# Performance work log

Measured on AMD Instinct MI355X. Metric: run time of the kernel, lower is better.

## Reference

```python
import jax, jax.numpy as jnp
import numpy as np

N_NODES = 20000
N_EDGES = 640000
D = 128            # node feature dim
NUM_HEADS = 4      # = num_irreps of edge_sh (lmax=3, 0e+1o+2e+3o)
HEAD_DIM = D // NUM_HEADS
IR_DIMS = np.array([1, 3, 5, 7])  # dims of each irrep; sum = 16
AVG_NUM_NEIGHBORS = 32.0


def setup_inputs() -> dict:
    key = jax.random.key(0)
    ks = jax.random.split(key, 20)
    inp = {
        "edge_sh": jax.random.normal(ks[0], (N_EDGES, int(IR_DIMS.sum())), jnp.float32),
        "node_feats": jax.random.normal(ks[1], (N_NODES, D), jnp.float32),
        "edge_feats": jax.random.normal(ks[2], (N_EDGES, 64), jnp.float32),
        "chi_scalar": jax.random.normal(ks[3], (N_EDGES, 64), jnp.float32),
        "cutoffs": jax.random.uniform(ks[4], (N_EDGES,), jnp.float32),
        "senders": jax.random.randint(ks[5], (N_EDGES,), 0, N_NODES),
        "receivers": jax.random.randint(ks[6], (N_EDGES,), 0, N_NODES),
        # radial MLP: 64 -> 128 -> 128 (silu between)
        "W_rad1": jax.random.normal(ks[7], (64, 128), jnp.float32) / np.sqrt(64),
        "b_rad1": jnp.zeros((128,), jnp.float32),
        "W_rad2": jax.random.normal(ks[8], (128, 128), jnp.float32) / np.sqrt(128),
        "b_rad2": jnp.zeros((128,), jnp.float32),
        # spherical-scalar MLP: 64 -> 128 -> 128
        "W_sph1": jax.random.normal(ks[9], (64, 128), jnp.float32) / np.sqrt(64),
        "b_sph1": jnp.zeros((128,), jnp.float32),
        "W_sph2": jax.random.normal(ks[10], (128, 128), jnp.float32) / np.sqrt(128),
        "b_sph2": jnp.zeros((128,), jnp.float32),
        # Q/K projections, no bias
        "Wq": jax.random.normal(ks[11], (D, D), jnp.float32) / np.sqrt(D),
        "Wk": jax.random.normal(ks[12], (D, D), jnp.float32) / np.sqrt(D),
    }
    return inp


def reference(edge_sh, node_feats, edge_feats, chi_scalar, cutoffs, senders,
              receivers, W_rad1, b_rad1, W_rad2, b_rad2, W_sph1, b_sph1,
              W_sph2, b_sph2, Wq, Wk):
    silu = jax.nn.silu
    # edge filter: radial MLP + spherical-scalar MLP
    w = silu(edge_feats @ W_rad1 + b_rad1) @ W_rad2 + b_rad2      # [E, D]
    w = w + (silu(chi_scalar @ W_sph1 + b_sph1) @ W_sph2 + b_sph2)
    w = w.reshape(-1, NUM_HEADS, HEAD_DIM)                        # [E, H, hd]
    # gathered queries/keys
    q = (node_feats @ Wq).reshape(-1, NUM_HEADS, HEAD_DIM)[receivers]
    k = (node_feats @ Wk).reshape(-1, NUM_HEADS, HEAD_DIM)[senders]
    # filter-scaled attention: per-edge, per-head scalar
    alpha = (q * w * k).sum(axis=-1) * (1.0 / np.sqrt(HEAD_DIM))  # [E, H]
    alpha = alpha * cutoffs[:, None]
    # aligned_mul: broadcast per-irrep weight over each irrep's dim (mul=1)
    y = jnp.repeat(alpha, IR_DIMS, axis=-1)                       # [E, 16]
    msg = edge_sh * y
    # scatter_sum into receivers
    chi = jax.ops.segment_sum(msg, receivers, num_segments=N_NODES)
    return chi / AVG_NUM_NEIGHBORS
```

## Files before the change

kernel.cpp:

```cpp
#include <hip/hip_runtime.h>
#include <cmath>

#define NNODES 20000
#define NEDGES 640000
#define DDIM   128
#define TN     16
#define BE     64

typedef __attribute__((ext_vector_type(8))) short bf16x8;
typedef __attribute__((ext_vector_type(4))) float f32x4;
typedef __attribute__((ext_vector_type(4))) unsigned short us4;
typedef __attribute__((ext_vector_type(8))) unsigned short us8;

__device__ __forceinline__ unsigned short f2bf(float x) {
    union { float f; unsigned u; } v; v.f = x;
    unsigned r = v.u + 0x7FFFu + ((v.u >> 16) & 1u);
    return (unsigned short)(r >> 16);
}
__device__ __forceinline__ float bf2f(unsigned short h) {
    union { unsigned u; float f; } v; v.u = ((unsigned)h) << 16; return v.f;
}
__device__ __forceinline__ unsigned cvtpk(float lo, float hi) {
    unsigned r;
    asm("v_cvt_pk_bf16_f32 %0, %1, %2" : "=v"(r) : "v"(lo), "v"(hi));
    return r;
}

__global__ void pack_weights(const float* __restrict__ W, unsigned short* __restrict__ dst)
{
    const int f  = blockIdx.x;
    const int kt = f >> 3, nt = f & 7;
    const int t  = threadIdx.x;
#pragma unroll
    for (int ii = 0; ii < 2; ii++) {
        const int idx  = t * 2 + ii;
        const int lane = idx >> 3, i = idx & 7;
        const int k = kt * 32 + (lane >> 4) * 8 + i;
        const int n = nt * 16 + (lane & 15);
        dst[f * 512 + idx] = f2bf(W[k * 128 + n]);
    }
}

__global__ __launch_bounds__(256) void qk_proj_kernel(
    const float* __restrict__ nf, const float* __restrict__ Wq,
    const float* __restrict__ Wk, unsigned short* __restrict__ qbuf,
    unsigned short* __restrict__ kbuf)
{
    __shared__ float s_nf[TN * DDIM];
    const int t  = threadIdx.x;
    const int n0 = blockIdx.x * TN;
    {
        const float4* src = (const float4*)(nf + (size_t)n0 * DDIM);
        float4* dst = (float4*)s_nf;
        for (int i = t; i < TN * DDIM / 4; i += 256) dst[i] = src[i];
    }
    __syncthreads();

    const int j = t & 127;
    const float* W = (t < 128) ? Wq : Wk;
    float acc[TN];
#pragma unroll
    for (int n = 0; n < TN; n++) acc[n] = 0.f;

    for (int k = 0; k < DDIM; k += 4) {
        const float w0 = W[(k + 0) * DDIM + j];
        const float w1 = W[(k + 1) * DDIM + j];
        const float w2 = W[(k + 2) * DDIM + j];
        const float w3 = W[(k + 3) * DDIM + j];
#pragma unroll
        for (int n = 0; n < TN; n++) {
            const float4 f = *(const float4*)&s_nf[n * DDIM + k];
            acc[n] = fmaf(f.w, w3, fmaf(f.z, w2, fmaf(f.y, w1, fmaf(f.x, w0, acc[n]))));
        }
    }
    unsigned short* outp = (t < 128) ? qbuf : kbuf;
    for (int n = 0; n < TN; n++) outp[(size_t)(n0 + n) * DDIM + j] = f2bf(acc[n]);
}

__global__ __launch_bounds__(256) void p_gather(
    const int* __restrict__ recv, const int* __restrict__ send,
    const unsigned short* __restrict__ qbuf, const unsigned short* __restrict__ kbuf,
    unsigned short* __restrict__ pedge)
{
    const int gid = blockIdx.x * 256 + threadIdx.x;
    const int e = gid >> 4;
    const int j = gid & 15;
    const int r = recv[e];
    const int s = send[e];
    const us8 qv = *(const us8*)(qbuf + (size_t)r * 128 + j * 8);
    const us8 kv = *(const us8*)(kbuf + (size_t)s * 128 + j * 8);
    uint4 pv;
    pv.x = cvtpk(bf2f(qv[0]) * bf2f(kv[0]), bf2f(qv[1]) * bf2f(kv[1]));
    pv.y = cvtpk(bf2f(qv[2]) * bf2f(kv[2]), bf2f(qv[3]) * bf2f(kv[3]));
    pv.z = cvtpk(bf2f(qv[4]) * bf2f(kv[4]), bf2f(qv[5]) * bf2f(kv[5]));
    pv.w = cvtpk(bf2f(qv[6]) * bf2f(kv[6]), bf2f(qv[7]) * bf2f(kv[7]));
    *(uint4*)(pedge + (size_t)e * 128 + j * 8) = pv;
}

__global__ __launch_bounds__(256, 4) void edge_kernel_v2(
    const float* __restrict__ edge_sh, const float* __restrict__ cutoffs,
    const int* __restrict__ receivers,
    const float* __restrict__ edge_feats, const float* __restrict__ chi_scalar,
    const unsigned short* __restrict__ w1r, const unsigned short* __restrict__ w1s,
    const unsigned short* __restrict__ w2r, const unsigned short* __restrict__ w2s,
    const float* __restrict__ b_rad1, const float* __restrict__ b_sph1,
    const float* __restrict__ b_rad2, const float* __restrict__ b_sph2,
    const unsigned short* __restrict__ pedge,
    float* __restrict__ out)
{
    __shared__ unsigned short s_a[2 * 64 * 64];
    __shared__ unsigned short s_h[64 * 128];
    __shared__ float s_alpha[64][4];
    char* pa = (char*)s_a;
    char* ph = (char*)s_h;

    const int t  = threadIdx.x;
    const int w  = t >> 6;
    const int l  = t & 63;
    const int el = l & 15;
    const int rg = l >> 4;
    const int eb = blockIdx.x * BE;

#pragma unroll
    for (int ii = 0; ii < 4; ii++) {
        const int idx = t + ii * 256;
        const int r   = idx >> 4;
        const int c4  = idx & 15;
        const float4 a = *(const float4*)(edge_feats + (size_t)(eb + r) * 64 + c4 * 4);
        const float4 b = *(const float4*)(chi_scalar + (size_t)(eb + r) * 64 + c4 * 4);
        const uint2 av = { cvtpk(a.x, a.y), cvtpk(a.z, a.w) };
        const uint2 bv = { cvtpk(b.x, b.y), cvtpk(b.z, b.w) };
        const int off = (r * 128 + c4 * 8) ^ ((r & 7) << 4);
        *(uint2*)(pa + off)        = av;
        *(uint2*)(pa + 8192 + off) = bv;
    }
    __syncthreads();

    f32x4 acc2[2][4];
#pragma unroll
    for (int ct = 0; ct < 2; ct++)
#pragma unroll
        for (int et = 0; et < 4; et++)
            acc2[ct][et] = (f32x4){0.f, 0.f, 0.f, 0.f};

#pragma unroll
    for (int path = 0; path < 2; path++) {
        const unsigned short* W1p = path ? w1s : w1r;
        const unsigned short* W2p = path ? w2s : w2r;
        const float* b1p = path ? b_sph1 : b_rad1;
        const char*  ab  = pa + path * 8192;

        f32x4 acc1[2][4];
#pragma unroll
        for (int ht = 0; ht < 2; ht++)
#pragma unroll
            for (int et = 0; et < 4; et++)
                acc1[ht][et] = (f32x4){0.f, 0.f, 0.f, 0.f};

#pragma unroll
        for (int kt = 0; kt < 2; kt++) {
            bf16x8 bfrag[4];
#pragma unroll
            for (int et = 0; et < 4; et++) {
                const int e = et * 16 + el;
                const int k = kt * 32 + rg * 8;
                bfrag[et] = *(const bf16x8*)(ab + ((e * 128 + k * 2) ^ ((e & 7) << 4)));
            }
#pragma unroll
            for (int ht = 0; ht < 2; ht++) {
                const int f = kt * 8 + (w * 2 + ht);
                const bf16x8 afrag = *(const bf16x8*)(W1p + (size_t)f * 512 + l * 8);
#pragma unroll
                for (int et = 0; et < 4; et++)
                    acc1[ht][et] = __builtin_amdgcn_mfma_f32_16x16x32_bf16(
                        afrag, bfrag[et], acc1[ht][et], 0, 0, 0);
            }
        }

#pragma unroll
        for (int ht = 0; ht < 2; ht++) {
            const int hid0 = w * 32 + ht * 16 + rg * 4;
            const float4 bv = *(const float4*)(b1p + hid0);
            const float* bvf = (const float*)&bv;
#pragma unroll
            for (int et = 0; et < 4; et++) {
                const int e = et * 16 + el;
                float s[4];
#pragma unroll
                for (int r = 0; r < 4; r++) {
                    const float v = acc1[ht][et][r] + bvf[r];
                    s[r] = v * __builtin_amdgcn_rcpf(1.0f + __expf(-v));
                }
                const uint2 hv = { cvtpk(s[0], s[1]), cvtpk(s[2], s[3]) };
                *(uint2*)(ph + ((e * 256 + hid0 * 2) ^ ((e & 7) << 4))) = hv;
            }
        }
        __syncthreads();

#pragma unroll
        for (int kt = 0; kt < 4; kt++) {
            bf16x8 hfrag[4];
#pragma unroll
            for (int et = 0; et < 4; et++) {
                const int e = et * 16 + el;
                const int k = kt * 32 + rg * 8;
                hfrag[et] = *(const bf16x8*)(ph + ((e * 256 + k * 2) ^ ((e & 7) << 4)));
            }
#pragma unroll
            for (int ct = 0; ct < 2; ct++) {
                const int f = kt * 8 + (w * 2 + ct);
                const bf16x8 afrag = *(const bf16x8*)(W2p + (size_t)f * 512 + l * 8);
#pragma unroll
                for (int et = 0; et < 4; et++)
                    acc2[ct][et] = __builtin_amdgcn_mfma_f32_16x16x32_bf16(
                        afrag, hfrag[et], acc2[ct][et], 0, 0, 0);
            }
        }
        if (path == 0) __syncthreads();
    }

    {
        const int c0base = w * 32 + rg * 4;
        f32x4 b2s[2];
#pragma unroll
        for (int ct = 0; ct < 2; ct++) {
            const float4 br = *(const float4*)(b_rad2 + c0base + ct * 16);
            const float4 bs = *(const float4*)(b_sph2 + c0base + ct * 16);
            b2s[ct] = (f32x4){ br.x + bs.x, br.y + bs.y, br.z + bs.z, br.w + bs.w };
        }
        us4 pv[2][4];
#pragma unroll
        for (int et = 0; et < 4; et++)
#pragma unroll
            for (int ct = 0; ct < 2; ct++)
                pv[ct][et] = *(const us4*)(pedge + (size_t)(eb + et * 16 + el) * 128
                                           + c0base + ct * 16);
#pragma unroll
        for (int et = 0; et < 4; et++) {
            float vsum = 0.f;
#pragma unroll
            for (int ct = 0; ct < 2; ct++) {
#pragma unroll
                for (int r = 0; r < 4; r++)
                    vsum = fmaf(bf2f(pv[ct][et][r]), acc2[ct][et][r] + b2s[ct][r], vsum);
            }
            vsum += __shfl_xor(vsum, 16, 64);
            vsum += __shfl_xor(vsum, 32, 64);
            if (l < 16) {
                s_alpha[et * 16 + l][w] = vsum * cutoffs[eb + et * 16 + l]
                                        * 0.005524271728019903f;
            }
        }
    }
    __syncthreads();

    {
        const int e   = t >> 2;
        const int c0q = t & 3;
        const int eg  = eb + e;
        const int rv  = receivers[eg];
        const float4 sh = *(const float4*)(edge_sh + (size_t)eg * 16 + c0q * 4);
        const float* shf = (const float*)&sh;
#pragma unroll
        for (int j = 0; j < 4; j++) {
            const int comp = c0q * 4 + j;
            const int head = (comp == 0) ? 0 : (comp < 4) ? 1 : (comp < 9) ? 2 : 3;
            atomicAdd(&out[(size_t)rv * 16 + comp], shf[j] * s_alpha[e][head]);
        }
    }
}

__global__ __launch_bounds__(256) void edge_kernel_fb(
    const float* __restrict__ edge_sh, const float* __restrict__ cutoffs,
    const int* __restrict__ senders, const int* __restrict__ receivers,
    const float* __restrict__ edge_feats, const float* __restrict__ chi_scalar,
    const unsigned short* __restrict__ w1r, const unsigned short* __restrict__ w1s,
    const unsigned short* __restrict__ w2r, const unsigned short* __restrict__ w2s,
    const float* __restrict__ b_rad1, const float* __restrict__ b_sph1,
    const float* __restrict__ b_rad2, const float* __restrict__ b_sph2,
    const unsigned short* __restrict__ qbuf, const unsigned short* __restrict__ kbuf,
    float* __restrict__ out)
{
    __shared__ unsigned short s_a[2 * 64 * 64];
    __shared__ unsigned short s_h[64 * 128];
    __shared__ unsigned short s_p[64 * 128];
    __shared__ float s_alpha[64][4];
    char* pa = (char*)s_a;
    char* ph = (char*)s_h;
    char* pp = (char*)s_p;

    const int t  = threadIdx.x;
    const int w  = t >> 6;
    const int l  = t & 63;
    const int eb = blockIdx.x * BE;

#pragma unroll
    for (int ii = 0; ii < 8; ii++) {
        const int e  = w * 16 + ii * 2 + (l >> 5);
        const int eg = eb + e;
        const int r  = receivers[eg];
        const int s  = senders[eg];
        const int c4 = l & 31;
        const us4 qv = *(const us4*)(qbuf + (size_t)r * 128 + c4 * 4);
        const us4 kv = *(const us4*)(kbuf + (size_t)s * 128 + c4 * 4);
        const uint2 pv = { cvtpk(bf2f(qv[0]) * bf2f(kv[0]), bf2f(qv[1]) * bf2f(kv[1])),
                           cvtpk(bf2f(qv[2]) * bf2f(kv[2]), bf2f(qv[3]) * bf2f(kv[3])) };
        *(uint2*)(pp + ((e * 256 + c4 * 8) ^ ((e & 7) << 4))) = pv;
    }
#pragma unroll
    for (int ii = 0; ii < 4; ii++) {
        const int idx = t + ii * 256;
        const int r   = idx >> 4;
        const int c4  = idx & 15;
        const float4 a = *(const float4*)(edge_feats + (size_t)(eb + r) * 64 + c4 * 4);
        const float4 b = *(const float4*)(chi_scalar + (size_t)(eb + r) * 64 + c4 * 4);
        const uint2 av = { cvtpk(a.x, a.y), cvtpk(a.z, a.w) };
        const uint2 bv = { cvtpk(b.x, b.y), cvtpk(b.z, b.w) };
        const int off = (r * 128 + c4 * 8) ^ ((r & 7) << 4);
        *(uint2*)(pa + off)        = av;
        *(uint2*)(pa + 8192 + off) = bv;
    }
    __syncthreads();

    f32x4 acc2[2][4];
#pragma unroll
    for (int ct = 0; ct < 2; ct++)
#pragma unroll
        for (int et = 0; et < 4; et++)
            acc2[ct][et] = (f32x4){0.f, 0.f, 0.f, 0.f};

#pragma unroll
    for (int path = 0; path < 2; path++) {
        const unsigned short* W1p = path ? w1s : w1r;
        const unsigned short* W2p = path ? w2s : w2r;
        const float* b1p = path ? b_sph1 : b_rad1;
        const char*  ab  = pa + path * 8192;

        f32x4 acc1[2][4];
#pragma unroll
        for (int ht = 0; ht < 2; ht++)
#pragma unroll
            for (int et = 0; et < 4; et++)
                acc1[ht][et] = (f32x4){0.f, 0.f, 0.f, 0.f};

#pragma unroll
        for (int kt = 0; kt < 2; kt++) {
            bf16x8 bfrag[4];
#pragma unroll
            for (int et = 0; et < 4; et++) {
                const int e = et * 16 + (l & 15);
                const int k = kt * 32 + (l >> 4) * 8;
                bfrag[et] = *(const bf16x8*)(ab + ((e * 128 + k * 2) ^ ((e & 7) << 4)));
            }
#pragma unroll
            for (int ht = 0; ht < 2; ht++) {
                const int f = kt * 8 + (w * 2 + ht);
                const bf16x8 afrag = *(const bf16x8*)(W1p + (size_t)f * 512 + l * 8);
#pragma unroll
                for (int et = 0; et < 4; et++)
                    acc1[ht][et] = __builtin_amdgcn_mfma_f32_16x16x32_bf16(
                        afrag, bfrag[et], acc1[ht][et], 0, 0, 0);
            }
        }
#pragma unroll
        for (int ht = 0; ht < 2; ht++) {
            const int hid0 = w * 32 + ht * 16 + (l >> 4) * 4;
            const float4 bv = *(const float4*)(b1p + hid0);
            const float* bvf = (const float*)&bv;
#pragma unroll
            for (int et = 0; et < 4; et++) {
                const int e = et * 16 + (l & 15);
                float s[4];
#pragma unroll
                for (int r = 0; r < 4; r++) {
                    const float v = acc1[ht][et][r] + bvf[r];
                    s[r] = v * __builtin_amdgcn_rcpf(1.0f + __expf(-v));
                }
                const uint2 hv = { cvtpk(s[0], s[1]), cvtpk(s[2], s[3]) };
                *(uint2*)(ph + ((e * 256 + hid0 * 2) ^ ((e & 7) << 4))) = hv;
            }
        }
        __syncthreads();

#pragma unroll
        for (int kt = 0; kt < 4; kt++) {
            bf16x8 hfrag[4];
#pragma unroll
            for (int et = 0; et < 4; et++) {
                const int e = et * 16 + (l & 15);
                const int k = kt * 32 + (l >> 4) * 8;
                hfrag[et] = *(const bf16x8*)(ph + ((e * 256 + k * 2) ^ ((e & 7) << 4)));
            }
#pragma unroll
            for (int ct = 0; ct < 2; ct++) {
                const int f = kt * 8 + (w * 2 + ct);
                const bf16x8 afrag = *(const bf16x8*)(W2p + (size_t)f * 512 + l * 8);
#pragma unroll
                for (int et = 0; et < 4; et++)
                    acc2[ct][et] = __builtin_amdgcn_mfma_f32_16x16x32_bf16(
                        afrag, hfrag[et], acc2[ct][et], 0, 0, 0);
            }
        }
        if (path == 0) __syncthreads();
    }

    {
        f32x4 b2s[2];
#pragma unroll
        for (int ct = 0; ct < 2; ct++) {
            const int c0 = w * 32 + ct * 16 + (l >> 4) * 4;
            const float4 br = *(const float4*)(b_rad2 + c0);
            const float4 bs = *(const float4*)(b_sph2 + c0);
            b2s[ct] = (f32x4){ br.x + bs.x, br.y + bs.y, br.z + bs.z, br.w + bs.w };
        }
#pragma unroll
        for (int et = 0; et < 4; et++) {
            const int e = et * 16 + (l & 15);
            float vsum = 0.f;
#pragma unroll
            for (int ct = 0; ct < 2; ct++) {
                const int c0 = w * 32 + ct * 16 + (l >> 4) * 4;
                const us4 pv = *(const us4*)(pp + ((e * 256 + c0 * 2) ^ ((e & 7) << 4)));
#pragma unroll
                for (int r = 0; r < 4; r++)
                    vsum = fmaf(bf2f(pv[r]), acc2[ct][et][r] + b2s[ct][r], vsum);
            }
            vsum += __shfl_xor(vsum, 16, 64);
            vsum += __shfl_xor(vsum, 32, 64);
            if (l < 16) {
                s_alpha[et * 16 + l][w] = vsum * cutoffs[eb + et * 16 + l]
                                        * 0.005524271728019903f;
            }
        }
    }
    __syncthreads();

    {
        const int e   = t >> 2;
        const int c0q = t & 3;
        const int eg  = eb + e;
        const int rn  = receivers[eg];
        const float4 sh = *(const float4*)(edge_sh + (size_t)eg * 16 + c0q * 4);
        const float* shf = (const float*)&sh;
#pragma unroll
        for (int j = 0; j < 4; j++) {
            const int comp = c0q * 4 + j;
            const int head = (comp == 0) ? 0 : (comp < 4) ? 1 : (comp < 9) ? 2 : 3;
            atomicAdd(&out[(size_t)rn * 16 + comp], shf[j] * s_alpha[e][head]);
        }
    }
}

extern "C" void kernel_launch(void* const* d_in, const int* in_sizes, int n_in,
                              void* d_out, int out_size, void* d_ws, size_t ws_size,
                              hipStream_t stream)
{
    const float* edge_sh    = (const float*)d_in[0];
    const float* node_feats = (const float*)d_in[1];
    const float* edge_feats = (const float*)d_in[2];
    const float* chi_scalar = (const float*)d_in[3];
    const float* cutoffs    = (const float*)d_in[4];
    const int*   senders    = (const int*)d_in[5];
    const int*   receivers  = (const int*)d_in[6];
    const float* W_rad1 = (const float*)d_in[7];
    const float* b_rad1 = (const float*)d_in[8];
    const float* W_rad2 = (const float*)d_in[9];
    const float* b_rad2 = (const float*)d_in[10];
    const float* W_sph1 = (const float*)d_in[11];
    const float* b_sph1 = (const float*)d_in[12];
    const float* W_sph2 = (const float*)d_in[13];
    const float* b_sph2 = (const float*)d_in[14];
    const float* Wq     = (const float*)d_in[15];
    const float* Wk     = (const float*)d_in[16];

    float* out = (float*)d_out;
    unsigned short* qbuf = (unsigned short*)d_ws;
    unsigned short* kbuf = qbuf + (size_t)NNODES * DDIM;
    unsigned short* w1r  = kbuf + (size_t)NNODES * DDIM;
    unsigned short* w1s  = w1r + 16 * 512;
    unsigned short* w2r  = w1s + 16 * 512;
    unsigned short* w2s  = w2r + 32 * 512;
    unsigned short* pedge = w2s + 32 * 512;

    const size_t need = ((size_t)((char*)pedge - (char*)d_ws))
                      + (size_t)NEDGES * DDIM * sizeof(unsigned short);
    const bool big = (ws_size >= need);

    hipMemsetAsync(out, 0, (size_t)out_size * sizeof(float), stream);

    pack_weights<<<16, 256, 0, stream>>>(W_rad1, w1r);
    pack_weights<<<16, 256, 0, stream>>>(W_sph1, w1s);
    pack_weights<<<32, 256, 0, stream>>>(W_rad2, w2r);
    pack_weights<<<32, 256, 0, stream>>>(W_sph2, w2s);

    qk_proj_kernel<<<NNODES / TN, 256, 0, stream>>>(node_feats, Wq, Wk, qbuf, kbuf);

    if (big) {
        p_gather<<<NEDGES * 16 / 256, 256, 0, stream>>>(receivers, senders, qbuf, kbuf, pedge);
        edge_kernel_v2<<<NEDGES / BE, 256, 0, stream>>>(
            edge_sh, cutoffs, receivers, edge_feats, chi_scalar,
            w1r, w1s, w2r, w2s, b_rad1, b_sph1, b_rad2, b_sph2,
            pedge, out);
    } else {
        edge_kernel_fb<<<NEDGES / BE, 256, 0, stream>>>(
            edge_sh, cutoffs, senders, receivers, edge_feats, chi_scalar,
            w1r, w1s, w2r, w2s, b_rad1, b_sph1, b_rad2, b_sph2,
            qbuf, kbuf, out);
    }
}
```

Before: 353.2 us.

## Split edge MLP from attention; fuse gather, dot and scatter into one kernel

The pipeline used to be a q*k product gather into an edge buffer followed by an MLP kernel that read it back and scattered. It now runs an MLP-only kernel that writes the bf16 edge filter, then one kernel that gathers q and k, dots them with the filter, reduces per head with shuffles, and atomically scatters the messages. The edge-sized intermediate is still written and read once, so buffer traffic is about the same. The atomics now come from a flat per-edge layout with 16 lanes per edge instead of after a block-level sync.

```diff
diff --git a/kernel.cpp b/kernel.cpp
--- a/kernel.cpp
+++ b/kernel.cpp
@@ -77,40 +77,16 @@
     for (int n = 0; n < TN; n++) outp[(size_t)(n0 + n) * DDIM + j] = f2bf(acc[n]);
 }
 
-__global__ __launch_bounds__(256) void p_gather(
-    const int* __restrict__ recv, const int* __restrict__ send,
-    const unsigned short* __restrict__ qbuf, const unsigned short* __restrict__ kbuf,
-    unsigned short* __restrict__ pedge)
-{
-    const int gid = blockIdx.x * 256 + threadIdx.x;
-    const int e = gid >> 4;
-    const int j = gid & 15;
-    const int r = recv[e];
-    const int s = send[e];
-    const us8 qv = *(const us8*)(qbuf + (size_t)r * 128 + j * 8);
-    const us8 kv = *(const us8*)(kbuf + (size_t)s * 128 + j * 8);
-    uint4 pv;
-    pv.x = cvtpk(bf2f(qv[0]) * bf2f(kv[0]), bf2f(qv[1]) * bf2f(kv[1]));
-    pv.y = cvtpk(bf2f(qv[2]) * bf2f(kv[2]), bf2f(qv[3]) * bf2f(kv[3]));
-    pv.z = cvtpk(bf2f(qv[4]) * bf2f(kv[4]), bf2f(qv[5]) * bf2f(kv[5]));
-    pv.w = cvtpk(bf2f(qv[6]) * bf2f(kv[6]), bf2f(qv[7]) * bf2f(kv[7]));
-    *(uint4*)(pedge + (size_t)e * 128 + j * 8) = pv;
-}
-
-__global__ __launch_bounds__(256, 4) void edge_kernel_v2(
-    const float* __restrict__ edge_sh, const float* __restrict__ cutoffs,
-    const int* __restrict__ receivers,
+__global__ __launch_bounds__(256, 4) void mlp_kernel(
     const float* __restrict__ edge_feats, const float* __restrict__ chi_scalar,
     const unsigned short* __restrict__ w1r, const unsigned short* __restrict__ w1s,
     const unsigned short* __restrict__ w2r, const unsigned short* __restrict__ w2s,
     const float* __restrict__ b_rad1, const float* __restrict__ b_sph1,
     const float* __restrict__ b_rad2, const float* __restrict__ b_sph2,
-    const unsigned short* __restrict__ pedge,
-    float* __restrict__ out)
+    unsigned short* __restrict__ wfilt)
 {
     __shared__ unsigned short s_a[2 * 64 * 64];
     __shared__ unsigned short s_h[64 * 128];
-    __shared__ float s_alpha[64][4];
     char* pa = (char*)s_a;
     char* ph = (char*)s_h;
 
@@ -221,53 +197,57 @@
 
     {
         const int c0base = w * 32 + rg * 4;
-        f32x4 b2s[2];
 #pragma unroll
         for (int ct = 0; ct < 2; ct++) {
             const float4 br = *(const float4*)(b_rad2 + c0base + ct * 16);
             const float4 bs = *(const float4*)(b_sph2 + c0base + ct * 16);
-            b2s[ct] = (f32x4){ br.x + bs.x, br.y + bs.y, br.z + bs.z, br.w + bs.w };
-        }
-        us4 pv[2][4];
-#pragma unroll
-        for (int et = 0; et < 4; et++)
-#pragma unroll
-            for (int ct = 0; ct < 2; ct++)
-                pv[ct][et] = *(const us4*)(pedge + (size_t)(eb + et * 16 + el) * 128
-                                           + c0base + ct * 16);
-#pragma unroll
-        for (int et = 0; et < 4; et++) {
-            float vsum = 0.f;
-#pragma unroll
-            for (int ct = 0; ct < 2; ct++) {
-#pragma unroll
-                for (int r = 0; r < 4; r++)
-                    vsum = fmaf(bf2f(pv[ct][et][r]), acc2[ct][et][r] + b2s[ct][r], vsum);
-            }
-            vsum += __shfl_xor(vsum, 16, 64);
-            vsum += __shfl_xor(vsum, 32, 64);
-            if (l < 16) {
-                s_alpha[et * 16 + l][w] = vsum * cutoffs[eb + et * 16 + l]
-                                        * 0.005524271728019903f;
-            }
-        }
-    }
-    __syncthreads();
-
-    {
-        const int e   = t >> 2;
-        const int c0q = t & 3;
-        const int eg  = eb + e;
-        const int rv  = receivers[eg];
-        const float4 sh = *(const float4*)(edge_sh + (size_t)eg * 16 + c0q * 4);
-        const float* shf = (const float*)&sh;
-#pragma unroll
-        for (int j = 0; j < 4; j++) {
-            const int comp = c0q * 4 + j;
-            const int head = (comp == 0) ? 0 : (comp < 4) ? 1 : (comp < 9) ? 2 : 3;
-            atomicAdd(&out[(size_t)rv * 16 + comp], shf[j] * s_alpha[e][head]);
-        }
-    }
+#pragma unroll
+            for (int et = 0; et < 4; et++) {
+                const float v0 = acc2[ct][et][0] + br.x + bs.x;
+                const float v1 = acc2[ct][et][1] + br.y + bs.y;
+                const float v2 = acc2[ct][et][2] + br.z + bs.z;
+                const float v3 = acc2[ct][et][3] + br.w + bs.w;
+                const uint2 wv = { cvtpk(v0, v1), cvtpk(v2, v3) };
+                const size_t e = eb + et * 16 + el;
+                *(uint2*)(wfilt + e * 128 + c0base + ct * 16) = wv;
+            }
+        }
+    }
+}
+
+__global__ __launch_bounds__(256) void attn_scatter(
+    const int* __restrict__ recv, const int* __restrict__ send,
+    const unsigned short* __restrict__ qbuf, const unsigned short* __restrict__ kbuf,
+    const unsigned short* __restrict__ wfilt,
+    const float* __restrict__ edge_sh, const float* __restrict__ cutoffs,
+    float* __restrict__ out)
+{
+    const int gid  = blockIdx.x * 256 + threadIdx.x;
+    const int e    = gid >> 4;
+    const int j    = gid & 15;
+    const int lane = threadIdx.x & 63;
+
+    const int r = recv[e];
+    const int s = send[e];
+
+    const us8 qv = *(const us8*)(qbuf + (size_t)r * 128 + j * 8);
+    const us8 kv = *(const us8*)(kbuf + (size_t)s * 128 + j * 8);
+    const us8 wv = *(const us8*)(wfilt + (size_t)e * 128 + j * 8);
+
+    float sum = 0.f;
+#pragma unroll
+    for (int i = 0; i < 8; i++)
+        sum = fmaf(bf2f(qv[i]) * bf2f(kv[i]), bf2f(wv[i]), sum);
+
+    sum += __shfl_xor(sum, 1, 64);
+    sum += __shfl_xor(sum, 2, 64);
+    const float alpha = sum * cutoffs[e] * 0.005524271728019903f;
+
+    const int hj = (j == 0) ? 0 : (j < 4) ? 1 : (j < 9) ? 2 : 3;
+    const float a = __shfl(alpha, (lane & ~15) | (hj << 2), 64);
+
+    const float msg = edge_sh[(size_t)e * 16 + j] * a;
+    atomicAdd(&out[(size_t)r * 16 + j], msg);
 }
 
 __global__ __launch_bounds__(256) void edge_kernel_fb(
@@ -474,15 +454,15 @@
     const float* Wk     = (const float*)d_in[16];
 
     float* out = (float*)d_out;
-    unsigned short* qbuf = (unsigned short*)d_ws;
-    unsigned short* kbuf = qbuf + (size_t)NNODES * DDIM;
-    unsigned short* w1r  = kbuf + (size_t)NNODES * DDIM;
-    unsigned short* w1s  = w1r + 16 * 512;
-    unsigned short* w2r  = w1s + 16 * 512;
-    unsigned short* w2s  = w2r + 32 * 512;
-    unsigned short* pedge = w2s + 32 * 512;
-
-    const size_t need = ((size_t)((char*)pedge - (char*)d_ws))
+    unsigned short* qbuf  = (unsigned short*)d_ws;
+    unsigned short* kbuf  = qbuf + (size_t)NNODES * DDIM;
+    unsigned short* w1r   = kbuf + (size_t)NNODES * DDIM;
+    unsigned short* w1s   = w1r + 16 * 512;
+    unsigned short* w2r   = w1s + 16 * 512;
+    unsigned short* w2s   = w2r + 32 * 512;
+    unsigned short* wfilt = w2s + 32 * 512;
+
+    const size_t need = (size_t)((char*)wfilt - (char*)d_ws)
                       + (size_t)NEDGES * DDIM * sizeof(unsigned short);
     const bool big = (ws_size >= need);
 
@@ -496,11 +476,11 @@
     qk_proj_kernel<<<NNODES / TN, 256, 0, stream>>>(node_feats, Wq, Wk, qbuf, kbuf);
 
     if (big) {
-        p_gather<<<NEDGES * 16 / 256, 256, 0, stream>>>(receivers, senders, qbuf, kbuf, pedge);
-        edge_kernel_v2<<<NEDGES / BE, 256, 0, stream>>>(
-            edge_sh, cutoffs, receivers, edge_feats, chi_scalar,
-            w1r, w1s, w2r, w2s, b_rad1, b_sph1, b_rad2, b_sph2,
-            pedge, out);
+        mlp_kernel<<<NEDGES / BE, 256, 0, stream>>>(
+            edge_feats, chi_scalar, w1r, w1s, w2r, w2s,
+            b_rad1, b_sph1, b_rad2, b_sph2, wfilt);
+        attn_scatter<<<NEDGES * 16 / 256, 256, 0, stream>>>(
+            receivers, senders, qbuf, kbuf, wfilt, edge_sh, cutoffs, out);
     } else {
         edge_kernel_fb<<<NEDGES / BE, 256, 0, stream>>>(
             edge_sh, cutoffs, senders, receivers, edge_feats, chi_scalar,
```

Result: faster. 300.2 us (-15.0%).
